# Kernel optimization log

Measured on AMD Instinct MI355X. Metric: run time of the kernel, lower is better.

The kernel has to match this reference:

```python
import jax, jax.numpy as jnp
jax.config.update("jax_enable_x64", True)
import numpy as np

N_E = 8192      # codebook size
E_DIM = 512     # code dim
BETA = 0.25
SK_EPS = 0.003
SK_ITERS = 5
N_TOK = 8192


def sinkhorn(d, eps, iters):
    # d: [B, K] centered distances in float64 (matches torch .double())
    Q = jnp.exp(-d / eps).T            # [K, B]
    K, B = Q.shape
    Q = Q / Q.sum()

    def body(Q, _):
        Q = Q / Q.sum(axis=1, keepdims=True) / K   # normalize rows (codes)
        Q = Q / Q.sum(axis=0, keepdims=True) / B   # normalize cols (tokens)
        return Q, None

    Q, _ = jax.lax.scan(body, Q, None, length=iters)
    Q = Q * B
    return Q.T                          # [B, K]


def setup_inputs() -> dict:
    key = jax.random.key(0)
    k1, k2 = jax.random.split(key)
    x = jax.random.normal(k1, (N_TOK, E_DIM), dtype=jnp.float32)
    # nn.Embedding weight init: uniform(-1/n_e, 1/n_e)
    emb = jax.random.uniform(k2, (N_E, E_DIM), dtype=jnp.float32,
                             minval=-1.0 / N_E, maxval=1.0 / N_E)
    return {"x": x, "emb": emb}


def reference(x, emb):
    latent = x.reshape(-1, E_DIM)                                  # [B, D]
    # pairwise squared L2: ||z||^2 + ||e||^2 - 2 z e^T  -> [B, K]
    d = (jnp.sum(latent ** 2, axis=1, keepdims=True)
         + jnp.sum(emb ** 2, axis=1)[None, :]
         - 2.0 * latent @ emb.T)
    # center_distance_for_constraint
    mx = d.max()
    mn = d.min()
    middle = (mx + mn) / 2
    amplitude = mx - middle + 1e-5
    dc = ((d - middle) / amplitude).astype(jnp.float64)
    Q = sinkhorn(dc, SK_EPS, SK_ITERS)
    indices = jnp.argmax(Q, axis=-1)                               # [B]
    x_q = emb[indices].reshape(x.shape)
    codebook_loss = jnp.mean((x_q - jax.lax.stop_gradient(x)) ** 2)
    commitment_loss = jnp.mean((jax.lax.stop_gradient(x_q) - x) ** 2)
    loss = codebook_loss + BETA * commitment_loss
    # straight-through estimator
    x_q_st = x + jax.lax.stop_gradient(x_q - x)
    return x_q_st, loss, indices.reshape(x.shape[:-1])
```

## Files before the change

kernel.cpp:

```cpp
#include <hip/hip_runtime.h>
#include <cfloat>
#include <cstdint>
#include <cstddef>

#define NTOK 8192
#define NE   8192
#define DIM  512
#define OUT0 4194304

#define EXPC64 92.332482616893656768
#define LN2HI64 1.0830424693267559631e-02
#define LN2LO64 2.9815858269852932812e-12
__device__ __forceinline__ double fexp_t(double x, const double* __restrict__ T){
  double nd = rint(x * EXPC64);
  double r  = fma(-nd, LN2HI64, x);
  r = fma(-nd, LN2LO64, r);
  double p = fma(r, 1.0/24.0, 1.0/6.0);
  p = fma(p, r, 0.5);
  p = fma(p, r, 1.0);
  p = fma(p, r, 1.0);
  int n = (int)nd;
  int j = n & 63;
  int e = n >> 6;
  long long eb = ((long long)(1023 + e)) << 52;
  return (T[j] * p) * __longlong_as_double(eb);
}
#define EXP_TABLE_INIT(Tbl) do{ \
    if (threadIdx.x < 64) Tbl[threadIdx.x] = exp2((double)threadIdx.x * 0.015625); \
    __syncthreads(); }while(0)

__device__ __forceinline__ unsigned int f2ord(float f){
  unsigned int u = __float_as_uint(f);
  return (u & 0x80000000u) ? ~u : (u | 0x80000000u);
}
__device__ __forceinline__ float ord2f(unsigned int v){
  unsigned int u = (v & 0x80000000u) ? (v ^ 0x80000000u) : ~v;
  return __uint_as_float(u);
}

__device__ float pw128_sq(const float* __restrict__ p){
  float r[8];
#pragma unroll
  for (int j = 0; j < 8; ++j) r[j] = __fmul_rn(p[j], p[j]);
#pragma unroll
  for (int i = 8; i < 128; i += 8)
#pragma unroll
    for (int j = 0; j < 8; ++j) r[j] = __fadd_rn(r[j], __fmul_rn(p[i+j], p[i+j]));
  float s01 = __fadd_rn(r[0], r[1]), s23 = __fadd_rn(r[2], r[3]);
  float s45 = __fadd_rn(r[4], r[5]), s67 = __fadd_rn(r[6], r[7]);
  return __fadd_rn(__fadd_rn(s01, s23), __fadd_rn(s45, s67));
}
__device__ float pw512_sq(const float* __restrict__ p){
  float s0 = __fadd_rn(pw128_sq(p),       pw128_sq(p + 128));
  float s1 = __fadd_rn(pw128_sq(p + 256), pw128_sq(p + 384));
  return __fadd_rn(s0, s1);
}

__global__ __launch_bounds__(256) void normsK(const float* __restrict__ X, const float* __restrict__ E,
    float* __restrict__ avec, float* __restrict__ hvec){
  int blk = blockIdx.x;
  int i = (blk & 31) * 256 + threadIdx.x;
  if (blk < 32) avec[i] = pw512_sq(X + (size_t)i * DIM);
  else          hvec[i] = pw512_sq(E + (size_t)i * DIM);
}

__global__ void initK(unsigned int* sc32){
  if (threadIdx.x == 0){ sc32[0] = 0u; sc32[1] = 0xFFFFFFFFu; }
}

__global__ void finalizeK(const unsigned int* sc32, float* scf){
  if (threadIdx.x == 0){
    float mx = ord2f(sc32[0]);
    float mn = ord2f(sc32[1]);
    float middle = __fmul_rn(__fadd_rn(mx, mn), 0.5f);
    float amp    = __fadd_rn(__fsub_rn(mx, middle), 1e-5f);
    scf[0] = middle; scf[1] = amp;
  }
}

__global__ void diagK(float* __restrict__ out, int n, float tag){
  int i = blockIdx.x * blockDim.x + threadIdx.x;
  int stride = gridDim.x * blockDim.x;
  for (; i < n; i += stride) out[i] = (i == OUT0) ? tag : 0.f;
}

#define GBM 128
#define GBN 128
#define GBK 16
#define GLDT 132
__global__ __launch_bounds__(256, 4) void gemm128(const float* __restrict__ X, const float* __restrict__ E,
    const float* __restrict__ avec, const float* __restrict__ hvec,
    float* __restrict__ dmat, unsigned int* __restrict__ sc32){
  __shared__ float As[GBK][GLDT];
  __shared__ float Bs[GBK][GLDT];
  __shared__ float red[256];
  int tid = threadIdx.x;
  int tx = tid & 15, ty = tid >> 4;
  int bm = blockIdx.y * GBM, bn = blockIdx.x * GBN;

  float acc[2][4][2][4];
#pragma unroll
  for (int ih = 0; ih < 2; ++ih)
#pragma unroll
    for (int i = 0; i < 4; ++i)
#pragma unroll
      for (int jh = 0; jh < 2; ++jh)
#pragma unroll
        for (int j = 0; j < 4; ++j) acc[ih][i][jh][j] = 0.f;

  for (int kt = 0; kt < DIM; kt += GBK){
#pragma unroll
    for (int s = 0; s < 2; ++s){
      int flat = tid + s * 256;
      int m  = flat >> 2;
      int k4 = (flat & 3) * 4;
      float4 va = *(const float4*)(X + (size_t)(bm + m) * DIM + kt + k4);
      As[k4+0][m] = va.x; As[k4+1][m] = va.y; As[k4+2][m] = va.z; As[k4+3][m] = va.w;
      float4 vb = *(const float4*)(E + (size_t)(bn + m) * DIM + kt + k4);
      Bs[k4+0][m] = vb.x; Bs[k4+1][m] = vb.y; Bs[k4+2][m] = vb.z; Bs[k4+3][m] = vb.w;
    }
    __syncthreads();
#pragma unroll
    for (int kk = 0; kk < GBK; ++kk){
      float a[2][4], b[2][4];
      *(float4*)a[0] = *(const float4*)&As[kk][ty * 4];
      *(float4*)a[1] = *(const float4*)&As[kk][64 + ty * 4];
      *(float4*)b[0] = *(const float4*)&Bs[kk][tx * 4];
      *(float4*)b[1] = *(const float4*)&Bs[kk][64 + tx * 4];
#pragma unroll
      for (int ih = 0; ih < 2; ++ih)
#pragma unroll
        for (int i = 0; i < 4; ++i)
#pragma unroll
          for (int jh = 0; jh < 2; ++jh)
#pragma unroll
            for (int j = 0; j < 4; ++j)
              acc[ih][i][jh][j] = fmaf(a[ih][i], b[jh][j], acc[ih][i][jh][j]);
    }
    __syncthreads();
  }

  float lmax = -FLT_MAX, lmin = FLT_MAX;
#pragma unroll
  for (int ih = 0; ih < 2; ++ih){
#pragma unroll
    for (int i = 0; i < 4; ++i){
      int gr = bm + ih * 64 + ty * 4 + i;
      float a = avec[gr];
#pragma unroll
      for (int jh = 0; jh < 2; ++jh){
        float dv[4];
#pragma unroll
        for (int j = 0; j < 4; ++j){
          int gc = bn + jh * 64 + tx * 4 + j;
          float t = __fadd_rn(a, hvec[gc]);
          float d = __fsub_rn(t, 2.0f * acc[ih][i][jh][j]);
          dv[j] = d;
          lmax = fmaxf(lmax, d); lmin = fminf(lmin, d);
        }
        *(float4*)(dmat + (size_t)gr * NE + bn + jh * 64 + tx * 4) = *(float4*)&dv[0];
      }
    }
  }
  red[tid] = lmax; __syncthreads();
  for (int s = 128; s > 0; s >>= 1){ if (tid < s) red[tid] = fmaxf(red[tid], red[tid+s]); __syncthreads(); }
  float bmax = red[0];
  __syncthreads();
  red[tid] = lmin; __syncthreads();
  for (int s = 128; s > 0; s >>= 1){ if (tid < s) red[tid] = fminf(red[tid], red[tid+s]); __syncthreads(); }
  if (tid == 0){
    atomicMax(&sc32[0], f2ord(bmax));
    atomicMin(&sc32[1], f2ord(red[0]));
  }
}

#define EXPC(x) fexp_t((double)(x) * NIE, Tbl)

template<bool CONVERT>
__global__ __launch_bounds__(256) void rowPassK(float* __restrict__ dmat, const double* __restrict__ wvec,
    const float* __restrict__ scf, double* __restrict__ partials){
  __shared__ double Tbl[64];
  EXP_TABLE_INIT(Tbl);
  int tid = threadIdx.x;
  int k0 = (blockIdx.x * 256 + tid) * 4;
  int b0 = blockIdx.y * 64;
  const double NIE = -(1.0 / 0.003);
  float* p = dmat + (size_t)b0 * NE + k0;
  double a0 = 0.0, a1 = 0.0, a2 = 0.0, a3 = 0.0;
  if (CONVERT){
    float middle = scf[0], amp = scf[1];
    for (int bb = 0; bb < 64; ++bb){
      float4 v = *(const float4*)(p + (size_t)bb * NE);
      float c0 = __fdiv_rn(__fsub_rn(v.x, middle), amp);
      float c1 = __fdiv_rn(__fsub_rn(v.y, middle), amp);
      float c2 = __fdiv_rn(__fsub_rn(v.z, middle), amp);
      float c3 = __fdiv_rn(__fsub_rn(v.w, middle), amp);
      float4 w; w.x = c0; w.y = c1; w.z = c2; w.w = c3;
      *(float4*)(p + (size_t)bb * NE) = w;
      a0 += EXPC(c0); a1 += EXPC(c1); a2 += EXPC(c2); a3 += EXPC(c3);
    }
  } else {
    for (int bb = 0; bb < 64; bb += 2){
      float4 v0 = *(const float4*)(p + (size_t)(bb+0) * NE);
      float4 v1 = *(const float4*)(p + (size_t)(bb+1) * NE);
      double w0 = wvec[b0+bb+0], w1 = wvec[b0+bb+1];
      a0 = fma(EXPC(v0.x), w0, a0); a1 = fma(EXPC(v0.y), w0, a1);
      a2 = fma(EXPC(v0.z), w0, a2); a3 = fma(EXPC(v0.w), w0, a3);
      a0 = fma(EXPC(v1.x), w1, a0); a1 = fma(EXPC(v1.y), w1, a1);
      a2 = fma(EXPC(v1.z), w1, a2); a3 = fma(EXPC(v1.w), w1, a3);
    }
  }
  double* q = partials + (size_t)blockIdx.y * NE + k0;
  q[0] = a0; q[1] = a1; q[2] = a2; q[3] = a3;
}

template<bool WRITE_LNA>
__global__ void reduceAK(const double* __restrict__ partials, double* __restrict__ ak,
    double* __restrict__ lna){
  int k = blockIdx.x * 256 + threadIdx.x;
  double s = 0.0;
  for (int c = 0; c < 128; ++c) s += partials[(size_t)c * NE + k];
  double a = 1.0 / (8192.0 * s);
  ak[k] = a;
  if (WRITE_LNA) lna[k] = log(a);
}

__global__ __launch_bounds__(256) void colPassK(const float* __restrict__ dmat, const double* __restrict__ ak,
    double* __restrict__ bvec){
  __shared__ double Tbl[64];
  __shared__ double sd[256];
  EXP_TABLE_INIT(Tbl);
  int b = blockIdx.x, tid = threadIdx.x;
  const double NIE = -(1.0 / 0.003);
  const float* row = dmat + (size_t)b * NE;
  double c0 = 0.0, c1 = 0.0, c2 = 0.0, c3 = 0.0;
#pragma unroll 2
  for (int kb = 0; kb < 8; ++kb){
    int k = kb * 1024 + tid * 4;
    float4 v = *(const float4*)(row + k);
    double q0 = ak[k], q1 = ak[k+1], q2 = ak[k+2], q3 = ak[k+3];
    c0 = fma(EXPC(v.x), q0, c0);
    c1 = fma(EXPC(v.y), q1, c1);
    c2 = fma(EXPC(v.z), q2, c2);
    c3 = fma(EXPC(v.w), q3, c3);
  }
  sd[tid] = (c0 + c1) + (c2 + c3); __syncthreads();
  for (int s = 128; s > 0; s >>= 1){ if (tid < s) sd[tid] += sd[tid+s]; __syncthreads(); }
  if (tid == 0) bvec[b] = 1.0 / (8192.0 * sd[0]);
}

__global__ __launch_bounds__(256) void argmaxLossK(const float* __restrict__ dmat, const double* __restrict__ lna,
    const float* __restrict__ X, const float* __restrict__ E,
    float* __restrict__ idxF, double* __restrict__ lparts){
  __shared__ double sv[256];
  __shared__ int    si[256];
  __shared__ int    sidx;
  int b = blockIdx.x, tid = threadIdx.x;
  const double NIE = -(1.0 / 0.003);
  const float* row = dmat + (size_t)b * NE;
  double best = -1.0e300; int bk = NE;
#pragma unroll 2
  for (int c = 0; c < 8; ++c){
    int k = c * 1024 + tid * 4;
    float4 v = *(const float4*)(row + k);
    double l0 = lna[k], l1 = lna[k+1], l2 = lna[k+2], l3 = lna[k+3];
    double t0 = fma((double)v.x, NIE, l0);
    double t1 = fma((double)v.y, NIE, l1);
    double t2 = fma((double)v.z, NIE, l2);
    double t3 = fma((double)v.w, NIE, l3);
    if (t0 > best){ best = t0; bk = k; }
    if (t1 > best){ best = t1; bk = k+1; }
    if (t2 > best){ best = t2; bk = k+2; }
    if (t3 > best){ best = t3; bk = k+3; }
  }
  sv[tid] = best; si[tid] = bk; __syncthreads();
  for (int s = 128; s > 0; s >>= 1){
    if (tid < s){
      double o = sv[tid+s]; int ok = si[tid+s];
      if (o > sv[tid] || (o == sv[tid] && ok < si[tid])){ sv[tid] = o; si[tid] = ok; }
    }
    __syncthreads();
  }
  if (tid == 0){ idxF[b] = (float)si[0]; sidx = si[0]; }
  __syncthreads();

  int id = sidx;
  const float* xr = X + (size_t)b * DIM;
  const float* er = E + (size_t)id * DIM;
  double ls = 0.0;
#pragma unroll
  for (int c = 0; c < 2; ++c){
    int dpos = tid + c * 256;
    float diff = __fsub_rn(er[dpos], xr[dpos]);
    ls = fma((double)diff, (double)diff, ls);
  }
  sv[tid] = ls; __syncthreads();
  for (int s = 128; s > 0; s >>= 1){ if (tid < s) sv[tid] += sv[tid+s]; __syncthreads(); }
  if (tid == 0) lparts[b] = sv[0];
}

__global__ __launch_bounds__(256) void lossFinK(const double* __restrict__ lparts, float* __restrict__ lossOut){
  __shared__ double sd[256];
  int tid = threadIdx.x;
  double s = 0.0;
  for (int b = tid; b < NTOK; b += 256) s += lparts[b];
  sd[tid] = s; __syncthreads();
  for (int st = 128; st > 0; st >>= 1){ if (tid < st) sd[tid] += sd[tid+st]; __syncthreads(); }
  if (tid == 0){
    double v = sd[0] / (double)((size_t)NTOK * DIM);
    float vf = (float)v;
    lossOut[0] = __fadd_rn(vf, __fmul_rn(0.25f, vf));
  }
}

__global__ __launch_bounds__(256) void out0K(const float* __restrict__ X, const float* __restrict__ E,
    const float* __restrict__ idxF, float* __restrict__ out0){
  int b = blockIdx.x, tid = threadIdx.x;
  int id = (int)idxF[b];
  const float* xr = X + (size_t)b * DIM;
  const float* er = E + (size_t)id * DIM;
#pragma unroll
  for (int c = 0; c < 2; ++c){
    int dpos = tid + c * 256;
    float xv = xr[dpos];
    float diff = __fsub_rn(er[dpos], xv);
    out0[(size_t)b * DIM + dpos] = __fadd_rn(xv, diff);
  }
}

extern "C" void kernel_launch(void* const* d_in, const int* in_sizes, int n_in,
                              void* d_out, int out_size, void* d_ws, size_t ws_size,
                              hipStream_t stream){
  (void)in_sizes; (void)n_in;
  const float* X = (const float*)d_in[0];
  const float* E = (const float*)d_in[1];
  float* out = (float*)d_out;

  if (ws_size < 268435456ull || d_ws == nullptr){
    diagK<<<2048, 256, 0, stream>>>(out, out_size, (float)(ws_size >> 20));
    return;
  }
  float* dmat = (float*)d_ws;

  float*  avec   = out;
  float*  hvec   = out + 8192;
  double* parts  = (double*)(out + 16384);
  double* ak     = (double*)(out + 2113536);
  double* bvec   = (double*)(out + 2129920);
  double* lna    = (double*)(out + 2146304);
  unsigned int* sc32 = (unsigned int*)(out + 2162688);
  float*  scf    = out + 2162690;
  double* lparts = parts;

  float* out0    = out;
  float* lossOut = out + OUT0;
  float* idxF    = out + OUT0 + 1;

  initK<<<1, 64, 0, stream>>>(sc32);
  normsK<<<64, 256, 0, stream>>>(X, E, avec, hvec);

  dim3 gg(NE / GBN, NTOK / GBM);
  gemm128<<<gg, 256, 0, stream>>>(X, E, avec, hvec, dmat, sc32);
  finalizeK<<<1, 64, 0, stream>>>(sc32, scf);

  dim3 rp(8, 128);
  rowPassK<true><<<rp, 256, 0, stream>>>(dmat, nullptr, scf, parts);
  reduceAK<false><<<32, 256, 0, stream>>>(parts, ak, lna);
  for (int it = 0; it < 4; ++it){
    colPassK<<<NTOK, 256, 0, stream>>>(dmat, ak, bvec);
    rowPassK<false><<<rp, 256, 0, stream>>>(dmat, bvec, scf, parts);
    if (it < 3) reduceAK<false><<<32, 256, 0, stream>>>(parts, ak, lna);
    else        reduceAK<true ><<<32, 256, 0, stream>>>(parts, ak, lna);
  }

  argmaxLossK<<<NTOK, 256, 0, stream>>>(dmat, lna, X, E, idxF, lparts);
  lossFinK<<<1, 256, 0, stream>>>(lparts, lossOut);
  out0K<<<NTOK, 256, 0, stream>>>(X, E, idxF, out0);
}
```

Before: 1.425 ms.

## Fuse Sinkhorn column and row passes into one per-iteration kernel

Replaces the separate column-normalization kernel and the row-pass kernel with a single kernel. Each block walks 64 token rows, computes the exponentials once, reduces each row to its column scale with a block reduction, then accumulates the row partial sums in registers. This halves the number of full reads of the distance matrix per iteration and avoids computing the exponentials twice. In exchange it launches only 128 blocks, which leaves many CUs idle, and it adds a block-wide barrier for every row, so it may end up latency-bound.

```diff
diff --git a/kernel.cpp b/kernel.cpp
--- a/kernel.cpp
+++ b/kernel.cpp
@@ -214,6 +214,68 @@
   q[0] = a0; q[1] = a1; q[2] = a2; q[3] = a3;
 }
 
+__global__ __launch_bounds__(512, 2) void sinkIterK(const float* __restrict__ dmat,
+    const double* __restrict__ ak, double* __restrict__ partials){
+  __shared__ double Tbl[64];
+  __shared__ double ws[2][8];
+  if (threadIdx.x < 64) Tbl[threadIdx.x] = exp2((double)threadIdx.x * 0.015625);
+  __syncthreads();
+  int tid = threadIdx.x;
+  int b0 = blockIdx.x * 64;
+  const double NIE = -(1.0 / 0.003);
+
+  double akr[16];
+#pragma unroll
+  for (int kb = 0; kb < 4; ++kb){
+    int k = tid * 4 + kb * 2048;
+    akr[kb*4+0] = ak[k+0]; akr[kb*4+1] = ak[k+1];
+    akr[kb*4+2] = ak[k+2]; akr[kb*4+3] = ak[k+3];
+  }
+  double racc[16];
+#pragma unroll
+  for (int i = 0; i < 16; ++i) racc[i] = 0.0;
+
+  for (int r = 0; r < 64; ++r){
+    const float* rp = dmat + (size_t)(b0 + r) * NE;
+    float4 v[4];
+#pragma unroll
+    for (int kb = 0; kb < 4; ++kb) v[kb] = *(const float4*)(rp + tid * 4 + kb * 2048);
+    double e[16];
+#pragma unroll
+    for (int kb = 0; kb < 4; ++kb){
+      e[kb*4+0] = EXPC(v[kb].x); e[kb*4+1] = EXPC(v[kb].y);
+      e[kb*4+2] = EXPC(v[kb].z); e[kb*4+3] = EXPC(v[kb].w);
+    }
+    double s0 = 0.0, s1 = 0.0, s2 = 0.0, s3 = 0.0;
+#pragma unroll
+    for (int kb = 0; kb < 4; ++kb){
+      s0 = fma(e[kb*4+0], akr[kb*4+0], s0);
+      s1 = fma(e[kb*4+1], akr[kb*4+1], s1);
+      s2 = fma(e[kb*4+2], akr[kb*4+2], s2);
+      s3 = fma(e[kb*4+3], akr[kb*4+3], s3);
+    }
+    double s = (s0 + s1) + (s2 + s3);
+#pragma unroll
+    for (int m = 1; m < 64; m <<= 1) s += __shfl_xor(s, m, 64);
+    int par = r & 1;
+    if ((tid & 63) == 0) ws[par][tid >> 6] = s;
+    __syncthreads();
+    double c = ((ws[par][0] + ws[par][1]) + (ws[par][2] + ws[par][3]))
+             + ((ws[par][4] + ws[par][5]) + (ws[par][6] + ws[par][7]));
+    double bb = 1.0 / (8192.0 * c);
+#pragma unroll
+    for (int i = 0; i < 16; ++i) racc[i] = fma(e[i], bb, racc[i]);
+  }
+
+  double* q = partials + (size_t)blockIdx.x * NE;
+#pragma unroll
+  for (int kb = 0; kb < 4; ++kb){
+    int k = tid * 4 + kb * 2048;
+    q[k+0] = racc[kb*4+0]; q[k+1] = racc[kb*4+1];
+    q[k+2] = racc[kb*4+2]; q[k+3] = racc[kb*4+3];
+  }
+}
+
 template<bool WRITE_LNA>
 __global__ void reduceAK(const double* __restrict__ partials, double* __restrict__ ak,
     double* __restrict__ lna){
@@ -223,30 +285,6 @@
   double a = 1.0 / (8192.0 * s);
   ak[k] = a;
   if (WRITE_LNA) lna[k] = log(a);
-}
-
-__global__ __launch_bounds__(256) void colPassK(const float* __restrict__ dmat, const double* __restrict__ ak,
-    double* __restrict__ bvec){
-  __shared__ double Tbl[64];
-  __shared__ double sd[256];
-  EXP_TABLE_INIT(Tbl);
-  int b = blockIdx.x, tid = threadIdx.x;
-  const double NIE = -(1.0 / 0.003);
-  const float* row = dmat + (size_t)b * NE;
-  double c0 = 0.0, c1 = 0.0, c2 = 0.0, c3 = 0.0;
-#pragma unroll 2
-  for (int kb = 0; kb < 8; ++kb){
-    int k = kb * 1024 + tid * 4;
-    float4 v = *(const float4*)(row + k);
-    double q0 = ak[k], q1 = ak[k+1], q2 = ak[k+2], q3 = ak[k+3];
-    c0 = fma(EXPC(v.x), q0, c0);
-    c1 = fma(EXPC(v.y), q1, c1);
-    c2 = fma(EXPC(v.z), q2, c2);
-    c3 = fma(EXPC(v.w), q3, c3);
-  }
-  sd[tid] = (c0 + c1) + (c2 + c3); __syncthreads();
-  for (int s = 128; s > 0; s >>= 1){ if (tid < s) sd[tid] += sd[tid+s]; __syncthreads(); }
-  if (tid == 0) bvec[b] = 1.0 / (8192.0 * sd[0]);
 }
 
 __global__ __launch_bounds__(256) void argmaxLossK(const float* __restrict__ dmat, const double* __restrict__ lna,
@@ -351,6 +389,7 @@
   unsigned int* sc32 = (unsigned int*)(out + 2162688);
   float*  scf    = out + 2162690;
   double* lparts = parts;
+  (void)bvec;
 
   float* out0    = out;
   float* lossOut = out + OUT0;
@@ -367,8 +406,7 @@
   rowPassK<true><<<rp, 256, 0, stream>>>(dmat, nullptr, scf, parts);
   reduceAK<false><<<32, 256, 0, stream>>>(parts, ak, lna);
   for (int it = 0; it < 4; ++it){
-    colPassK<<<NTOK, 256, 0, stream>>>(dmat, ak, bvec);
-    rowPassK<false><<<rp, 256, 0, stream>>>(dmat, bvec, scf, parts);
+    sinkIterK<<<128, 512, 0, stream>>>(dmat, ak, parts);
     if (it < 3) reduceAK<false><<<32, 256, 0, stream>>>(parts, ak, lna);
     else        reduceAK<true ><<<32, 256, 0, stream>>>(parts, ak, lna);
   }
```

Result: slower. 1.591 ms (+11.7%).
